# Kernel optimization log

Measured on AMD Instinct MI355X. Metric: run time of the kernel, lower is better.

The kernel has to match this reference:

```python
import jax, jax.numpy as jnp
import numpy as np

VOCAB = 50000
D_EMB = 300
N_BINS = 11
B, LQ, LD = 64, 32, 1024
MU = np.array([1.0, 0.9, 0.7, 0.5, 0.3, 0.1, -0.1, -0.3, -0.5, -0.7, -0.9], dtype=np.float32)
SIGMA = np.array([1e-3] + [0.1] * 10, dtype=np.float32)


def setup_inputs() -> dict:
    key = jax.random.key(0)
    ks = jax.random.split(key, 8)
    inputs_q = jax.random.randint(ks[0], (B, LQ), 0, VOCAB, dtype=jnp.int64 if jax.config.jax_enable_x64 else jnp.int32)
    inputs_d = jax.random.randint(ks[1], (B, LD), 0, VOCAB, dtype=jnp.int64 if jax.config.jax_enable_x64 else jnp.int32)
    mask_q = jnp.ones((B, LQ), dtype=jnp.float32)
    mask_d = jnp.ones((B, LD), dtype=jnp.float32)
    word_emb = jax.random.normal(ks[2], (VOCAB, D_EMB), dtype=jnp.float32) * 0.1
    attn_table = jax.random.uniform(ks[3], (VOCAB, 1), dtype=jnp.float32)  # frozen IDF embedding
    idf_w = jax.random.normal(ks[4], (1, 1), dtype=jnp.float32)
    idf_b = jnp.zeros((1,), dtype=jnp.float32)
    dense_w = jax.random.normal(ks[5], (1, N_BINS), dtype=jnp.float32) * 0.1
    dense_b = jnp.zeros((1,), dtype=jnp.float32)
    return {
        'inputs_q': inputs_q, 'inputs_d': inputs_d,
        'mask_q': mask_q, 'mask_d': mask_d,
        'word_emb': word_emb, 'attn_table': attn_table,
        'idf_w': idf_w, 'idf_b': idf_b,
        'dense_w': dense_w, 'dense_b': dense_b,
    }


def _l2_normalize(x, eps=1e-12):
    # matches F.normalize(x, 2, dim=-1): x / max(||x||, eps)
    n = jnp.sqrt(jnp.sum(x * x, axis=-1, keepdims=True))
    return x / jnp.maximum(n, eps)


def reference(inputs_q, inputs_d, mask_q, mask_d, word_emb, attn_table,
              idf_w, idf_b, dense_w, dense_b):
    mu = jnp.asarray(MU)        # [K]
    sigma = jnp.asarray(SIGMA)  # [K]
    # idf attention on query tokens: Linear(1,1) on frozen embedding lookup
    attn_q = attn_table[inputs_q] * idf_w[0, 0] + idf_b[0]          # [B,Lq,1]
    q_embed = _l2_normalize(word_emb[inputs_q])                      # [B,Lq,E]
    d_embed = _l2_normalize(word_emb[inputs_d])                      # [B,Ld,E]
    sim = jnp.einsum('bqe,bde->bqd', q_embed, d_embed)               # [B,Lq,Ld]
    # RBF soft-histogram over n_bins kernels, doc tokens masked
    rbf = jnp.exp(-((sim[..., None] - mu) ** 2) / (sigma ** 2) / 2)  # [B,Lq,Ld,K]
    pooling_sum = jnp.einsum('bqdk,bd->bqk', rbf, mask_d)            # [B,Lq,K]
    wq = mask_q[..., None] * attn_q                                   # [B,Lq,1]
    log_pool = jnp.log(jnp.clip(pooling_sum, 1e-10)) * wq * 0.01     # [B,Lq,K]
    log_pooling_sum = jnp.sum(log_pool, axis=1)                      # [B,K]
    out = jnp.tanh(log_pooling_sum @ dense_w.T + dense_b)            # [B,1]
    return out[:, 0]                                                 # [B]
```

## Files before the change

### kernel.cpp

```cpp
#include <hip/hip_runtime.h>
#include <math.h>

#define VOCAB  50000
#define D_EMB  300
#define NBINS  11
#define BATCH  64
#define LQ     32
#define LD     1024
#define DTILE  64
#define NDT    (LD / DTILE)
#define NSTEP  10

typedef __attribute__((ext_vector_type(8))) short short8;
typedef __attribute__((ext_vector_type(4))) float floatx4;

__constant__ float c_mu[NBINS]  = {1.0f, 0.9f, 0.7f, 0.5f, 0.3f, 0.1f,
                                   -0.1f, -0.3f, -0.5f, -0.7f, -0.9f};
__constant__ float c_is2[NBINS] = {500000.0f, 50.f, 50.f, 50.f, 50.f, 50.f,
                                   50.f, 50.f, 50.f, 50.f, 50.f};

static __device__ __forceinline__ unsigned short f32_bf16(float f) {
  unsigned u = __float_as_uint(f);
  u += 0x7FFFu + ((u >> 16) & 1u);
  return (unsigned short)(u >> 16);
}
static __device__ __forceinline__ float bf16_f32(unsigned short h) {
  return __uint_as_float(((unsigned)h) << 16);
}

static __device__ __forceinline__ float stage_rows(
    const float* __restrict__ emb_row,
    short* __restrict__ region,
    int s_begin, int s_end, int khi, int lane)
{
  const float4* emb4 = (const float4*)emb_row;
  float p = 0.f;
  for (int s = s_begin; s < s_end; ++s) {
    const int k0 = 32 * s + 8 * khi;
    float4 fa = make_float4(0.f, 0.f, 0.f, 0.f);
    float4 fb = make_float4(0.f, 0.f, 0.f, 0.f);
    if (k0 < D_EMB)     fa = emb4[k0 >> 2];
    if (k0 + 4 < D_EMB) fb = emb4[(k0 >> 2) + 1];
    unsigned short h[8];
    h[0] = f32_bf16(fa.x); h[1] = f32_bf16(fa.y);
    h[2] = f32_bf16(fa.z); h[3] = f32_bf16(fa.w);
    h[4] = f32_bf16(fb.x); h[5] = f32_bf16(fb.y);
    h[6] = f32_bf16(fb.z); h[7] = f32_bf16(fb.w);
    short8 v;
#pragma unroll
    for (int j = 0; j < 8; ++j) {
      const float x = bf16_f32(h[j]);
      p += x * x;
      v[j] = (short)h[j];
    }
    *(short8*)(region + s * 512 + lane * 8) = v;
  }
  return p;
}

__global__ __launch_bounds__(256) void knrm_main(
    const int* __restrict__ inputs_q, const int* __restrict__ inputs_d,
    const float* __restrict__ mask_d, const float* __restrict__ word_emb,
    float* __restrict__ partial)
{
  const int b    = blockIdx.y;
  const int dt   = blockIdx.x;
  const int tid  = threadIdx.x;
  const int wid  = tid >> 6;
  const int lane = tid & 63;
  const int khi  = lane >> 4;
  const int rl   = lane & 15;

  __shared__ __align__(16) short Afrag[2 * NSTEP * 512];
  __shared__ __align__(16) short Bfrag[4 * NSTEP * 512];
  __shared__ float sumsq_s[96];
  __shared__ float invq_s[LQ], invd_s[DTILE], maskd_s[DTILE];
  __shared__ float red[4][16][NBINS];

  if (tid < 96) sumsq_s[tid] = 0.f;
  if (tid < DTILE) maskd_s[tid] = mask_d[b * LD + dt * DTILE + tid];
  __syncthreads();

  {
    int tok; float p;
    if (wid == 0) {
      tok = inputs_q[b * LQ + rl];
      p = stage_rows(word_emb + (size_t)tok * D_EMB, Afrag, 0, NSTEP, khi, lane);
      p += __shfl_xor(p, 16); p += __shfl_xor(p, 32);
      if (lane < 16) atomicAdd(&sumsq_s[lane], p);
      tok = inputs_d[b * LD + dt * DTILE + rl];
      p = stage_rows(word_emb + (size_t)tok * D_EMB, Bfrag, 0, 5, khi, lane);
      p += __shfl_xor(p, 16); p += __shfl_xor(p, 32);
      if (lane < 16) atomicAdd(&sumsq_s[32 + lane], p);
    } else if (wid == 1) {
      tok = inputs_q[b * LQ + 16 + rl];
      p = stage_rows(word_emb + (size_t)tok * D_EMB, Afrag + NSTEP * 512, 0, NSTEP, khi, lane);
      p += __shfl_xor(p, 16); p += __shfl_xor(p, 32);
      if (lane < 16) atomicAdd(&sumsq_s[16 + lane], p);
      tok = inputs_d[b * LD + dt * DTILE + rl];
      p = stage_rows(word_emb + (size_t)tok * D_EMB, Bfrag, 5, NSTEP, khi, lane);
      p += __shfl_xor(p, 16); p += __shfl_xor(p, 32);
      if (lane < 16) atomicAdd(&sumsq_s[32 + lane], p);
    } else if (wid == 2) {
      tok = inputs_d[b * LD + dt * DTILE + 16 + rl];
      p = stage_rows(word_emb + (size_t)tok * D_EMB, Bfrag + NSTEP * 512, 0, NSTEP, khi, lane);
      p += __shfl_xor(p, 16); p += __shfl_xor(p, 32);
      if (lane < 16) atomicAdd(&sumsq_s[48 + lane], p);
      tok = inputs_d[b * LD + dt * DTILE + 32 + rl];
      p = stage_rows(word_emb + (size_t)tok * D_EMB, Bfrag + 2 * NSTEP * 512, 0, 5, khi, lane);
      p += __shfl_xor(p, 16); p += __shfl_xor(p, 32);
      if (lane < 16) atomicAdd(&sumsq_s[64 + lane], p);
    } else {
      tok = inputs_d[b * LD + dt * DTILE + 48 + rl];
      p = stage_rows(word_emb + (size_t)tok * D_EMB, Bfrag + 3 * NSTEP * 512, 0, NSTEP, khi, lane);
      p += __shfl_xor(p, 16); p += __shfl_xor(p, 32);
      if (lane < 16) atomicAdd(&sumsq_s[80 + lane], p);
      tok = inputs_d[b * LD + dt * DTILE + 32 + rl];
      p = stage_rows(word_emb + (size_t)tok * D_EMB, Bfrag + 2 * NSTEP * 512, 5, NSTEP, khi, lane);
      p += __shfl_xor(p, 16); p += __shfl_xor(p, 32);
      if (lane < 16) atomicAdd(&sumsq_s[64 + lane], p);
    }
  }
  __syncthreads();

  if (tid < 96) {
    const float s   = sumsq_s[tid];
    const float inv = 1.f / fmaxf(sqrtf(s), 1e-12f);
    if (tid < 32) invq_s[tid] = inv; else invd_s[tid - 32] = inv;
  }
  __syncthreads();

  const int qt = wid >> 1, dp = wid & 1;
  const short* Ab = Afrag + qt * NSTEP * 512;
  const short* B0 = Bfrag + (2 * dp) * NSTEP * 512;
  const short* B1 = Bfrag + (2 * dp + 1) * NSTEP * 512;
  floatx4 acc0 = {0.f, 0.f, 0.f, 0.f};
  floatx4 acc1 = {0.f, 0.f, 0.f, 0.f};
#pragma unroll
  for (int s = 0; s < NSTEP; ++s) {
    const short8 a  = *(const short8*)(Ab + s * 512 + lane * 8);
    const short8 b0 = *(const short8*)(B0 + s * 512 + lane * 8);
    const short8 b1 = *(const short8*)(B1 + s * 512 + lane * 8);
    acc0 = __builtin_amdgcn_mfma_f32_16x16x32_bf16(a, b0, acc0, 0, 0, 0);
    acc1 = __builtin_amdgcn_mfma_f32_16x16x32_bf16(a, b1, acc1, 0, 0, 0);
  }

  float ps[4][NBINS];
#pragma unroll
  for (int r = 0; r < 4; ++r)
#pragma unroll
    for (int k = 0; k < NBINS; ++k) ps[r][k] = 0.f;

  float iq[4];
#pragma unroll
  for (int r = 0; r < 4; ++r) iq[r] = invq_s[16 * qt + 4 * khi + r];

#pragma unroll
  for (int t = 0; t < 2; ++t) {
    const int   dl = 32 * dp + 16 * t + rl;
    const float id = invd_s[dl];
    const float md = maskd_s[dl];
    const floatx4 acc = t ? acc1 : acc0;
#pragma unroll
    for (int r = 0; r < 4; ++r) {
      const float sv = acc[r] * iq[r] * id;
#pragma unroll
      for (int k = 0; k < NBINS; ++k) {
        const float d = sv - c_mu[k];
        ps[r][k] += md * __expf(-d * d * c_is2[k]);
      }
    }
  }

#pragma unroll
  for (int off = 1; off < 16; off <<= 1)
#pragma unroll
    for (int r = 0; r < 4; ++r)
#pragma unroll
      for (int k = 0; k < NBINS; ++k)
        ps[r][k] += __shfl_xor(ps[r][k], off);

  if (rl == 0)
#pragma unroll
    for (int r = 0; r < 4; ++r)
#pragma unroll
      for (int k = 0; k < NBINS; ++k)
        red[wid][4 * khi + r][k] = ps[r][k];
  __syncthreads();

  for (int v = tid; v < LQ * NBINS; v += 256) {
    const int q = v / NBINS, k = v % NBINS;
    const float sv = (q < 16) ? (red[0][q][k] + red[1][q][k])
                              : (red[2][q - 16][k] + red[3][q - 16][k]);
    partial[((size_t)(b * LQ + q) * NBINS + k) * NDT + dt] = sv;
  }
}

__global__ __launch_bounds__(128) void knrm_finalize(
    const float* __restrict__ partial, const int* __restrict__ inputs_q,
    const float* __restrict__ mask_q, const float* __restrict__ attn_table,
    const float* __restrict__ idf_w, const float* __restrict__ idf_b,
    const float* __restrict__ dense_w, const float* __restrict__ dense_b,
    float* __restrict__ out)
{
  const int b   = blockIdx.x;
  const int tid = threadIdx.x;
  __shared__ float pool[LQ][NBINS];
  __shared__ float wq_s[LQ];
  __shared__ float lps[NBINS];

  for (int v = tid; v < LQ * NBINS; v += 128) {
    const int q = v / NBINS, k = v % NBINS;
    const float* p = partial + ((size_t)(b * LQ + q) * NBINS + k) * NDT;
    float s = 0.f;
#pragma unroll
    for (int t = 0; t < NDT; ++t) s += p[t];
    pool[q][k] = logf(fmaxf(s, 1e-10f));
  }
  if (tid < LQ) {
    const int tok = inputs_q[b * LQ + tid];
    wq_s[tid] = mask_q[b * LQ + tid] * (attn_table[tok] * idf_w[0] + idf_b[0]);
  }
  __syncthreads();
  if (tid < NBINS) {
    float s = 0.f;
    for (int q = 0; q < LQ; ++q) s += pool[q][tid] * wq_s[q];
    lps[tid] = 0.01f * s;
  }
  __syncthreads();
  if (tid == 0) {
    float z = dense_b[0];
    for (int k = 0; k < NBINS; ++k) z += lps[k] * dense_w[k];
    out[b] = tanhf(z);
  }
}

extern "C" void kernel_launch(void* const* d_in, const int* in_sizes, int n_in,
                              void* d_out, int out_size, void* d_ws, size_t ws_size,
                              hipStream_t stream) {
  const int*   inputs_q  = (const int*)d_in[0];
  const int*   inputs_d  = (const int*)d_in[1];
  const float* mask_q    = (const float*)d_in[2];
  const float* mask_d    = (const float*)d_in[3];
  const float* word_emb  = (const float*)d_in[4];
  const float* attn_tab  = (const float*)d_in[5];
  const float* idf_w     = (const float*)d_in[6];
  const float* idf_b     = (const float*)d_in[7];
  const float* dense_w   = (const float*)d_in[8];
  const float* dense_b   = (const float*)d_in[9];
  float* out     = (float*)d_out;
  float* partial = (float*)d_ws;

  dim3 grid(NDT, BATCH);
  knrm_main<<<grid, 256, 0, stream>>>(inputs_q, inputs_d, mask_d, word_emb, partial);
  knrm_finalize<<<BATCH, 128, 0, stream>>>(partial, inputs_q, mask_q, attn_tab,
                                           idf_w, idf_b, dense_w, dense_b, out);
}
```

Before: 134.5 us.

## Pre-convert embedding table to padded bf16 and stage rows via direct-to-LDS loads

A new prep kernel converts the whole 50000x300 fp32 embedding table into a padded 320-wide bf16 table and precomputes an inverse L2 norm per row. The main kernel then copies pre-packed fragments straight into LDS with global_load_lds, so it no longer converts or sums squares per tile. The partial-sum layout becomes dt-major so both stores and finalize reads are coalesced. The cost is converting all 50000 rows (about 60MB read, 32MB written) on every call, while only around 68K tokens are actually gathered. The old path is kept as a fallback for when the workspace is too small.

```diff
diff --git a/kernel.cpp b/kernel.cpp
--- a/kernel.cpp
+++ b/kernel.cpp
@@ -10,9 +10,19 @@
 #define DTILE  64
 #define NDT    (LD / DTILE)
 #define NSTEP  10
+#define KPAD   320
+
+#define PARTIAL_BYTES ((size_t)NDT * BATCH * LQ * NBINS * 4)
+#define TB_OFF        PARTIAL_BYTES
+#define TB_BYTES      ((size_t)VOCAB * KPAD * 2)
+#define INV_OFF       (TB_OFF + TB_BYTES)
+#define INV_BYTES     ((size_t)VOCAB * 4)
+#define WS_NEED       (INV_OFF + INV_BYTES)
 
 typedef __attribute__((ext_vector_type(8))) short short8;
 typedef __attribute__((ext_vector_type(4))) float floatx4;
+typedef __attribute__((ext_vector_type(4))) unsigned short us4;
+typedef unsigned int u32;
 
 __constant__ float c_mu[NBINS]  = {1.0f, 0.9f, 0.7f, 0.5f, 0.3f, 0.1f,
                                    -0.1f, -0.3f, -0.5f, -0.7f, -0.9f};
@@ -28,9 +38,157 @@
   return __uint_as_float(((unsigned)h) << 16);
 }
 
+static __device__ __forceinline__ void gload_lds16(const void* g, void* l) {
+  __builtin_amdgcn_global_load_lds(
+      (__attribute__((address_space(1))) u32*)g,
+      (__attribute__((address_space(3))) u32*)l, 16, 0, 0);
+}
+
+__global__ __launch_bounds__(256) void knrm_prep(
+    const float* __restrict__ word_emb,
+    unsigned short* __restrict__ tb, float* __restrict__ invn)
+{
+  const int wid  = threadIdx.x >> 6;
+  const int lane = threadIdx.x & 63;
+  const int row  = blockIdx.x * 4 + wid;
+  if (row >= VOCAB) return;
+  const float4* src = (const float4*)(word_emb + (size_t)row * D_EMB);
+  const float4 a = src[lane];
+  float4 c = make_float4(0.f, 0.f, 0.f, 0.f);
+  if (lane < 11) c = src[64 + lane];
+  us4 ha, hc;
+  ha.x = f32_bf16(a.x); ha.y = f32_bf16(a.y);
+  ha.z = f32_bf16(a.z); ha.w = f32_bf16(a.w);
+  hc.x = f32_bf16(c.x); hc.y = f32_bf16(c.y);
+  hc.z = f32_bf16(c.z); hc.w = f32_bf16(c.w);
+  float p = 0.f;
+  { float x;
+    x = bf16_f32(ha.x); p += x * x;  x = bf16_f32(ha.y); p += x * x;
+    x = bf16_f32(ha.z); p += x * x;  x = bf16_f32(ha.w); p += x * x;
+    x = bf16_f32(hc.x); p += x * x;  x = bf16_f32(hc.y); p += x * x;
+    x = bf16_f32(hc.z); p += x * x;  x = bf16_f32(hc.w); p += x * x; }
+#pragma unroll
+  for (int off = 1; off < 64; off <<= 1) p += __shfl_xor(p, off);
+  unsigned short* orow = tb + (size_t)row * KPAD;
+  *(us4*)(orow + 4 * lane) = ha;
+  if (lane < 16) *(us4*)(orow + 256 + 4 * lane) = hc;
+  if (lane == 0) invn[row] = 1.f / fmaxf(sqrtf(p), 1e-12f);
+}
+
+__global__ __launch_bounds__(256) void knrm_main(
+    const int* __restrict__ inputs_q, const int* __restrict__ inputs_d,
+    const float* __restrict__ mask_d, const unsigned short* __restrict__ tb,
+    const float* __restrict__ invn, float* __restrict__ partial)
+{
+  const int b    = blockIdx.y;
+  const int dt   = blockIdx.x;
+  const int tid  = threadIdx.x;
+  const int wid  = tid >> 6;
+  const int lane = tid & 63;
+  const int khi  = lane >> 4;
+  const int rl   = lane & 15;
+
+  __shared__ __align__(16) short Afrag[2 * NSTEP * 512];
+  __shared__ __align__(16) short Bfrag[4 * NSTEP * 512];
+  __shared__ float invq_s[LQ], invd_s[DTILE], maskd_s[DTILE];
+  __shared__ float red[4][16][NBINS];
+
+  const int dbase = b * LD + dt * DTILE;
+
+  int tokX, tokY, ybase;
+  short *dstX, *dstY;
+  if (wid == 0)      { tokX = inputs_q[b * LQ + rl];        dstX = Afrag;
+                       tokY = inputs_d[dbase + rl];         dstY = Bfrag;                  ybase = 0; }
+  else if (wid == 1) { tokX = inputs_q[b * LQ + 16 + rl];   dstX = Afrag + NSTEP * 512;
+                       tokY = inputs_d[dbase + rl];         dstY = Bfrag;                  ybase = 5; }
+  else if (wid == 2) { tokX = inputs_d[dbase + 16 + rl];    dstX = Bfrag + NSTEP * 512;
+                       tokY = inputs_d[dbase + 32 + rl];    dstY = Bfrag + 2 * NSTEP * 512; ybase = 0; }
+  else               { tokX = inputs_d[dbase + 48 + rl];    dstX = Bfrag + 3 * NSTEP * 512;
+                       tokY = inputs_d[dbase + 32 + rl];    dstY = Bfrag + 2 * NSTEP * 512; ybase = 5; }
+
+  const char* srcX = (const char*)(tb + (size_t)tokX * KPAD) + khi * 16;
+  const char* srcY = (const char*)(tb + (size_t)tokY * KPAD) + khi * 16;
+#pragma unroll
+  for (int s = 0; s < NSTEP; ++s)
+    gload_lds16(srcX + 64 * s, dstX + s * 512);
+#pragma unroll
+  for (int s = 0; s < 5; ++s)
+    gload_lds16(srcY + 64 * (ybase + s), dstY + (ybase + s) * 512);
+
+  if (tid < LQ)      invq_s[tid] = invn[inputs_q[b * LQ + tid]];
+  else if (tid < 96) { const int d = tid - 32;
+                       invd_s[d]  = invn[inputs_d[dbase + d]];
+                       maskd_s[d] = mask_d[dbase + d]; }
+  __syncthreads();
+
+  const int qt = wid >> 1, dp = wid & 1;
+  const short* Ab = Afrag + qt * NSTEP * 512;
+  const short* B0 = Bfrag + (2 * dp) * NSTEP * 512;
+  const short* B1 = Bfrag + (2 * dp + 1) * NSTEP * 512;
+  floatx4 acc0 = {0.f, 0.f, 0.f, 0.f};
+  floatx4 acc1 = {0.f, 0.f, 0.f, 0.f};
+#pragma unroll
+  for (int s = 0; s < NSTEP; ++s) {
+    const short8 a  = *(const short8*)(Ab + s * 512 + lane * 8);
+    const short8 b0 = *(const short8*)(B0 + s * 512 + lane * 8);
+    const short8 b1 = *(const short8*)(B1 + s * 512 + lane * 8);
+    acc0 = __builtin_amdgcn_mfma_f32_16x16x32_bf16(a, b0, acc0, 0, 0, 0);
+    acc1 = __builtin_amdgcn_mfma_f32_16x16x32_bf16(a, b1, acc1, 0, 0, 0);
+  }
+
+  float ps[4][NBINS];
+#pragma unroll
+  for (int r = 0; r < 4; ++r)
+#pragma unroll
+    for (int k = 0; k < NBINS; ++k) ps[r][k] = 0.f;
+
+  float iq[4];
+#pragma unroll
+  for (int r = 0; r < 4; ++r) iq[r] = invq_s[16 * qt + 4 * khi + r];
+
+#pragma unroll
+  for (int t = 0; t < 2; ++t) {
+    const int   dl = 32 * dp + 16 * t + rl;
+    const float id = invd_s[dl];
+    const float md = maskd_s[dl];
+    const floatx4 acc = t ? acc1 : acc0;
+#pragma unroll
+    for (int r = 0; r < 4; ++r) {
+      const float sv = acc[r] * iq[r] * id;
+#pragma unroll
+      for (int k = 0; k < NBINS; ++k) {
+        const float d = sv - c_mu[k];
+        ps[r][k] += md * __expf(-d * d * c_is2[k]);
+      }
+    }
+  }
+
+#pragma unroll
+  for (int off = 1; off < 16; off <<= 1)
+#pragma unroll
+    for (int r = 0; r < 4; ++r)
+#pragma unroll
+      for (int k = 0; k < NBINS; ++k)
+        ps[r][k] += __shfl_xor(ps[r][k], off);
+
+  if (rl == 0)
+#pragma unroll
+    for (int r = 0; r < 4; ++r)
+#pragma unroll
+      for (int k = 0; k < NBINS; ++k)
+        red[wid][4 * khi + r][k] = ps[r][k];
+  __syncthreads();
+
+  float* pout = partial + ((size_t)dt * BATCH + b) * (LQ * NBINS);
+  for (int v = tid; v < LQ * NBINS; v += 256) {
+    const int q = v / NBINS, k = v % NBINS;
+    pout[v] = (q < 16) ? (red[0][q][k] + red[1][q][k])
+                       : (red[2][q - 16][k] + red[3][q - 16][k]);
+  }
+}
+
 static __device__ __forceinline__ float stage_rows(
-    const float* __restrict__ emb_row,
-    short* __restrict__ region,
+    const float* __restrict__ emb_row, short* __restrict__ region,
     int s_begin, int s_end, int khi, int lane)
 {
   const float4* emb4 = (const float4*)emb_row;
@@ -58,7 +216,7 @@
   return p;
 }
 
-__global__ __launch_bounds__(256) void knrm_main(
+__global__ __launch_bounds__(256) void knrm_main_fb(
     const int* __restrict__ inputs_q, const int* __restrict__ inputs_d,
     const float* __restrict__ mask_d, const float* __restrict__ word_emb,
     float* __restrict__ partial)
@@ -188,11 +346,11 @@
         red[wid][4 * khi + r][k] = ps[r][k];
   __syncthreads();
 
+  float* pout = partial + ((size_t)dt * BATCH + b) * (LQ * NBINS);
   for (int v = tid; v < LQ * NBINS; v += 256) {
     const int q = v / NBINS, k = v % NBINS;
-    const float sv = (q < 16) ? (red[0][q][k] + red[1][q][k])
-                              : (red[2][q - 16][k] + red[3][q - 16][k]);
-    partial[((size_t)(b * LQ + q) * NBINS + k) * NDT + dt] = sv;
+    pout[v] = (q < 16) ? (red[0][q][k] + red[1][q][k])
+                       : (red[2][q - 16][k] + red[3][q - 16][k]);
   }
 }
 
@@ -210,12 +368,11 @@
   __shared__ float lps[NBINS];
 
   for (int v = tid; v < LQ * NBINS; v += 128) {
-    const int q = v / NBINS, k = v % NBINS;
-    const float* p = partial + ((size_t)(b * LQ + q) * NBINS + k) * NDT;
     float s = 0.f;
 #pragma unroll
-    for (int t = 0; t < NDT; ++t) s += p[t];
-    pool[q][k] = logf(fmaxf(s, 1e-10f));
+    for (int t = 0; t < NDT; ++t)
+      s += partial[((size_t)t * BATCH + b) * (LQ * NBINS) + v];
+    pool[v / NBINS][v % NBINS] = logf(fmaxf(s, 1e-10f));
   }
   if (tid < LQ) {
     const int tok = inputs_q[b * LQ + tid];
@@ -252,7 +409,14 @@
   float* partial = (float*)d_ws;
 
   dim3 grid(NDT, BATCH);
-  knrm_main<<<grid, 256, 0, stream>>>(inputs_q, inputs_d, mask_d, word_emb, partial);
+  if (ws_size >= WS_NEED) {
+    unsigned short* tb = (unsigned short*)((char*)d_ws + TB_OFF);
+    float* invn        = (float*)((char*)d_ws + INV_OFF);
+    knrm_prep<<<VOCAB / 4, 256, 0, stream>>>(word_emb, tb, invn);
+    knrm_main<<<grid, 256, 0, stream>>>(inputs_q, inputs_d, mask_d, tb, invn, partial);
+  } else {
+    knrm_main_fb<<<grid, 256, 0, stream>>>(inputs_q, inputs_d, mask_d, word_emb, partial);
+  }
   knrm_finalize<<<BATCH, 128, 0, stream>>>(partial, inputs_q, mask_q, attn_tab,
                                            idf_w, idf_b, dense_w, dense_b, out);
 }
```

New measurement: 136.7 us. Within noise of the previous version (+1.6%).

## Load MFMA fragments directly into registers and halve doc tile per block

Applied to the files above, without the earlier changes.

The main kernel no longer stages bf16 fragments and norms through shared memory. Each wave loads its own query and doc rows straight into MFMA register fragments and computes row norms with shuffles. The doc tile shrinks from 64 to 32 so the grid doubles, and the partial buffer layout becomes contiguous per tile so both the writes and the finalize reads coalesce. In exchange, query rows are reloaded twice as often, register pressure rises from holding twenty short8 fragments, and finalize has twice as many partials to sum.

```diff
diff --git a/kernel.cpp b/kernel.cpp
--- a/kernel.cpp
+++ b/kernel.cpp
@@ -7,9 +7,11 @@
 #define BATCH  64
 #define LQ     32
 #define LD     1024
-#define DTILE  64
-#define NDT    (LD / DTILE)
 #define NSTEP  10
+#define DT2    32
+#define NDT2   (LD / DT2)
+
+#define PARTIAL2_BYTES ((size_t)NDT2 * BATCH * LQ * NBINS * 4)
 
 typedef __attribute__((ext_vector_type(8))) short short8;
 typedef __attribute__((ext_vector_type(4))) float floatx4;
@@ -28,37 +30,23 @@
   return __uint_as_float(((unsigned)h) << 16);
 }
 
-static __device__ __forceinline__ float stage_rows(
-    const float* __restrict__ emb_row,
-    short* __restrict__ region,
-    int s_begin, int s_end, int khi, int lane)
-{
-  const float4* emb4 = (const float4*)emb_row;
-  float p = 0.f;
-  for (int s = s_begin; s < s_end; ++s) {
-    const int k0 = 32 * s + 8 * khi;
-    float4 fa = make_float4(0.f, 0.f, 0.f, 0.f);
-    float4 fb = make_float4(0.f, 0.f, 0.f, 0.f);
-    if (k0 < D_EMB)     fa = emb4[k0 >> 2];
-    if (k0 + 4 < D_EMB) fb = emb4[(k0 >> 2) + 1];
-    unsigned short h[8];
-    h[0] = f32_bf16(fa.x); h[1] = f32_bf16(fa.y);
-    h[2] = f32_bf16(fa.z); h[3] = f32_bf16(fa.w);
-    h[4] = f32_bf16(fb.x); h[5] = f32_bf16(fb.y);
-    h[6] = f32_bf16(fb.z); h[7] = f32_bf16(fb.w);
-    short8 v;
+static __device__ __forceinline__ short8 cvt8(float4 fa, float4 fb, float& p) {
+  unsigned short h[8];
+  h[0] = f32_bf16(fa.x); h[1] = f32_bf16(fa.y);
+  h[2] = f32_bf16(fa.z); h[3] = f32_bf16(fa.w);
+  h[4] = f32_bf16(fb.x); h[5] = f32_bf16(fb.y);
+  h[6] = f32_bf16(fb.z); h[7] = f32_bf16(fb.w);
+  short8 v;
 #pragma unroll
-    for (int j = 0; j < 8; ++j) {
-      const float x = bf16_f32(h[j]);
-      p += x * x;
-      v[j] = (short)h[j];
-    }
-    *(short8*)(region + s * 512 + lane * 8) = v;
+  for (int j = 0; j < 8; ++j) {
+    const float x = bf16_f32(h[j]);
+    p += x * x;
+    v[j] = (short)h[j];
   }
-  return p;
+  return v;
 }
 
-__global__ __launch_bounds__(256) void knrm_main(
+__global__ __launch_bounds__(256) void knrm_main3(
     const int* __restrict__ inputs_q, const int* __restrict__ inputs_d,
     const float* __restrict__ mask_d, const float* __restrict__ word_emb,
     float* __restrict__ partial)
@@ -70,105 +58,59 @@
   const int lane = tid & 63;
   const int khi  = lane >> 4;
   const int rl   = lane & 15;
+  const int qt   = wid >> 1, dp = wid & 1;
 
-  __shared__ __align__(16) short Afrag[2 * NSTEP * 512];
-  __shared__ __align__(16) short Bfrag[4 * NSTEP * 512];
-  __shared__ float sumsq_s[96];
-  __shared__ float invq_s[LQ], invd_s[DTILE], maskd_s[DTILE];
   __shared__ float red[4][16][NBINS];
 
-  if (tid < 96) sumsq_s[tid] = 0.f;
-  if (tid < DTILE) maskd_s[tid] = mask_d[b * LD + dt * DTILE + tid];
-  __syncthreads();
+  const int dbase = b * LD + dt * DT2;
+  const int qtok  = inputs_q[b * LQ + qt * 16 + rl];
+  const int dtok  = inputs_d[dbase + dp * 16 + rl];
+  const float* qrow = word_emb + (size_t)qtok * D_EMB;
+  const float* drow = word_emb + (size_t)dtok * D_EMB;
 
-  {
-    int tok; float p;
-    if (wid == 0) {
-      tok = inputs_q[b * LQ + rl];
-      p = stage_rows(word_emb + (size_t)tok * D_EMB, Afrag, 0, NSTEP, khi, lane);
-      p += __shfl_xor(p, 16); p += __shfl_xor(p, 32);
-      if (lane < 16) atomicAdd(&sumsq_s[lane], p);
-      tok = inputs_d[b * LD + dt * DTILE + rl];
-      p = stage_rows(word_emb + (size_t)tok * D_EMB, Bfrag, 0, 5, khi, lane);
-      p += __shfl_xor(p, 16); p += __shfl_xor(p, 32);
-      if (lane < 16) atomicAdd(&sumsq_s[32 + lane], p);
-    } else if (wid == 1) {
-      tok = inputs_q[b * LQ + 16 + rl];
-      p = stage_rows(word_emb + (size_t)tok * D_EMB, Afrag + NSTEP * 512, 0, NSTEP, khi, lane);
-      p += __shfl_xor(p, 16); p += __shfl_xor(p, 32);
-      if (lane < 16) atomicAdd(&sumsq_s[16 + lane], p);
-      tok = inputs_d[b * LD + dt * DTILE + rl];
-      p = stage_rows(word_emb + (size_t)tok * D_EMB, Bfrag, 5, NSTEP, khi, lane);
-      p += __shfl_xor(p, 16); p += __shfl_xor(p, 32);
-      if (lane < 16) atomicAdd(&sumsq_s[32 + lane], p);
-    } else if (wid == 2) {
-      tok = inputs_d[b * LD + dt * DTILE + 16 + rl];
-      p = stage_rows(word_emb + (size_t)tok * D_EMB, Bfrag + NSTEP * 512, 0, NSTEP, khi, lane);
-      p += __shfl_xor(p, 16); p += __shfl_xor(p, 32);
-      if (lane < 16) atomicAdd(&sumsq_s[48 + lane], p);
-      tok = inputs_d[b * LD + dt * DTILE + 32 + rl];
-      p = stage_rows(word_emb + (size_t)tok * D_EMB, Bfrag + 2 * NSTEP * 512, 0, 5, khi, lane);
-      p += __shfl_xor(p, 16); p += __shfl_xor(p, 32);
-      if (lane < 16) atomicAdd(&sumsq_s[64 + lane], p);
-    } else {
-      tok = inputs_d[b * LD + dt * DTILE + 48 + rl];
-      p = stage_rows(word_emb + (size_t)tok * D_EMB, Bfrag + 3 * NSTEP * 512, 0, NSTEP, khi, lane);
-      p += __shfl_xor(p, 16); p += __shfl_xor(p, 32);
-      if (lane < 16) atomicAdd(&sumsq_s[80 + lane], p);
-      tok = inputs_d[b * LD + dt * DTILE + 32 + rl];
-      p = stage_rows(word_emb + (size_t)tok * D_EMB, Bfrag + 2 * NSTEP * 512, 5, NSTEP, khi, lane);
-      p += __shfl_xor(p, 16); p += __shfl_xor(p, 32);
-      if (lane < 16) atomicAdd(&sumsq_s[64 + lane], p);
-    }
-  }
-  __syncthreads();
-
-  if (tid < 96) {
-    const float s   = sumsq_s[tid];
-    const float inv = 1.f / fmaxf(sqrtf(s), 1e-12f);
-    if (tid < 32) invq_s[tid] = inv; else invd_s[tid - 32] = inv;
-  }
-  __syncthreads();
-
-  const int qt = wid >> 1, dp = wid & 1;
-  const short* Ab = Afrag + qt * NSTEP * 512;
-  const short* B0 = Bfrag + (2 * dp) * NSTEP * 512;
-  const short* B1 = Bfrag + (2 * dp + 1) * NSTEP * 512;
-  floatx4 acc0 = {0.f, 0.f, 0.f, 0.f};
-  floatx4 acc1 = {0.f, 0.f, 0.f, 0.f};
+  short8 afr[NSTEP], bfr[NSTEP];
+  float pq = 0.f, pd = 0.f;
 #pragma unroll
   for (int s = 0; s < NSTEP; ++s) {
-    const short8 a  = *(const short8*)(Ab + s * 512 + lane * 8);
-    const short8 b0 = *(const short8*)(B0 + s * 512 + lane * 8);
-    const short8 b1 = *(const short8*)(B1 + s * 512 + lane * 8);
-    acc0 = __builtin_amdgcn_mfma_f32_16x16x32_bf16(a, b0, acc0, 0, 0, 0);
-    acc1 = __builtin_amdgcn_mfma_f32_16x16x32_bf16(a, b1, acc1, 0, 0, 0);
+    const int k0 = 32 * s + 8 * khi;
+    float4 fa = make_float4(0.f, 0.f, 0.f, 0.f);
+    float4 fb = make_float4(0.f, 0.f, 0.f, 0.f);
+    if (k0 < D_EMB)     fa = *(const float4*)(qrow + k0);
+    if (k0 + 4 < D_EMB) fb = *(const float4*)(qrow + k0 + 4);
+    afr[s] = cvt8(fa, fb, pq);
   }
+#pragma unroll
+  for (int s = 0; s < NSTEP; ++s) {
+    const int k0 = 32 * s + 8 * khi;
+    float4 fa = make_float4(0.f, 0.f, 0.f, 0.f);
+    float4 fb = make_float4(0.f, 0.f, 0.f, 0.f);
+    if (k0 < D_EMB)     fa = *(const float4*)(drow + k0);
+    if (k0 + 4 < D_EMB) fb = *(const float4*)(drow + k0 + 4);
+    bfr[s] = cvt8(fa, fb, pd);
+  }
+  pq += __shfl_xor(pq, 16); pq += __shfl_xor(pq, 32);
+  pd += __shfl_xor(pd, 16); pd += __shfl_xor(pd, 32);
+  const float invq_own = 1.f / fmaxf(sqrtf(pq), 1e-12f);
+  const float invd     = 1.f / fmaxf(sqrtf(pd), 1e-12f);
 
-  float ps[4][NBINS];
+  floatx4 acc = {0.f, 0.f, 0.f, 0.f};
 #pragma unroll
-  for (int r = 0; r < 4; ++r)
-#pragma unroll
-    for (int k = 0; k < NBINS; ++k) ps[r][k] = 0.f;
+  for (int s = 0; s < NSTEP; ++s)
+    acc = __builtin_amdgcn_mfma_f32_16x16x32_bf16(afr[s], bfr[s], acc, 0, 0, 0);
 
   float iq[4];
 #pragma unroll
-  for (int r = 0; r < 4; ++r) iq[r] = invq_s[16 * qt + 4 * khi + r];
+  for (int r = 0; r < 4; ++r) iq[r] = __shfl(invq_own, 4 * khi + r);
 
+  const float md = mask_d[dbase + dp * 16 + rl];
+  float ps[4][NBINS];
 #pragma unroll
-  for (int t = 0; t < 2; ++t) {
-    const int   dl = 32 * dp + 16 * t + rl;
-    const float id = invd_s[dl];
-    const float md = maskd_s[dl];
-    const floatx4 acc = t ? acc1 : acc0;
+  for (int r = 0; r < 4; ++r) {
+    const float sv = acc[r] * iq[r] * invd;
 #pragma unroll
-    for (int r = 0; r < 4; ++r) {
-      const float sv = acc[r] * iq[r] * id;
-#pragma unroll
-      for (int k = 0; k < NBINS; ++k) {
-        const float d = sv - c_mu[k];
-        ps[r][k] += md * __expf(-d * d * c_is2[k]);
-      }
+    for (int k = 0; k < NBINS; ++k) {
+      const float d = sv - c_mu[k];
+      ps[r][k] = md * __expf(-d * d * c_is2[k]);
     }
   }
 
@@ -188,11 +130,11 @@
         red[wid][4 * khi + r][k] = ps[r][k];
   __syncthreads();
 
+  float* pout = partial + ((size_t)dt * BATCH + b) * (LQ * NBINS);
   for (int v = tid; v < LQ * NBINS; v += 256) {
     const int q = v / NBINS, k = v % NBINS;
-    const float sv = (q < 16) ? (red[0][q][k] + red[1][q][k])
-                              : (red[2][q - 16][k] + red[3][q - 16][k]);
-    partial[((size_t)(b * LQ + q) * NBINS + k) * NDT + dt] = sv;
+    pout[v] = (q < 16) ? (red[0][q][k] + red[1][q][k])
+                       : (red[2][q - 16][k] + red[3][q - 16][k]);
   }
 }
 
@@ -210,12 +152,11 @@
   __shared__ float lps[NBINS];
 
   for (int v = tid; v < LQ * NBINS; v += 128) {
-    const int q = v / NBINS, k = v % NBINS;
-    const float* p = partial + ((size_t)(b * LQ + q) * NBINS + k) * NDT;
     float s = 0.f;
 #pragma unroll
-    for (int t = 0; t < NDT; ++t) s += p[t];
-    pool[q][k] = logf(fmaxf(s, 1e-10f));
+    for (int t = 0; t < NDT2; ++t)
+      s += partial[((size_t)t * BATCH + b) * (LQ * NBINS) + v];
+    pool[v / NBINS][v % NBINS] = logf(fmaxf(s, 1e-10f));
   }
   if (tid < LQ) {
     const int tok = inputs_q[b * LQ + tid];
@@ -251,8 +192,8 @@
   float* out     = (float*)d_out;
   float* partial = (float*)d_ws;
 
-  dim3 grid(NDT, BATCH);
-  knrm_main<<<grid, 256, 0, stream>>>(inputs_q, inputs_d, mask_d, word_emb, partial);
+  dim3 grid(NDT2, BATCH);
+  knrm_main3<<<grid, 256, 0, stream>>>(inputs_q, inputs_d, mask_d, word_emb, partial);
   knrm_finalize<<<BATCH, 128, 0, stream>>>(partial, inputs_q, mask_q, attn_tab,
                                            idf_w, idf_b, dense_w, dense_b, out);
 }
```

Result: slower. 144.4 us (+7.4%).
